# Optimization experiments

Measured on AMD Instinct MI355X. Metric: run time of the kernel, lower is better.

Reference implementation:

```python
import jax, jax.numpy as jnp
import numpy as np

R, B, D, C = 64, 4096, 512, 128  # n_rules, batch, n_fea, n_cls


def setup_inputs() -> dict:
    key = jax.random.key(0)
    k0, k1, k2, k3, k4 = jax.random.split(key, 5)
    x = jax.random.normal(k0, (B, D), dtype=jnp.float32)
    proto = jax.random.normal(k1, (R, D), dtype=jnp.float32)
    var = jax.random.uniform(k2, (R, D), dtype=jnp.float32)
    W = jax.random.normal(k3, (R, D, C), dtype=jnp.float32) * 0.02
    b = jax.random.normal(k4, (R, C), dtype=jnp.float32) * 0.02
    return {"x": x, "proto": proto, "var": var, "W": W, "b": b}


def reference(x, proto, var, W, b):
    # Antecedent: Gaussian membership per rule, var clamped to [1e-4, 0.1]
    v = jnp.clip(var, 0.0001, 0.1)                                  # [R, D]
    diff = x[None, :, :] - proto[:, None, :]                        # [R, B, D]
    m = jnp.exp(-diff * diff / (2.0 * v[:, None, :] ** 2))          # [R, B, D]
    # Firing strength: sum of squared memberships over features, softmax over rules
    fs_ini = jnp.sum(m * m, axis=-1).T                              # [B, R]
    fire_strength = jax.nn.softmax(fs_ini, axis=1)                  # [B, R]
    # Consequent: per-rule Linear + ReLU (batched GEMM over rules)
    expert = jax.nn.relu(jnp.einsum('bd,rdc->rbc', x, W) + b[:, None, :])  # [R, B, C]
    # Softmax-weighted combine over rules
    out = jnp.einsum('rbc,br->bc', expert, fire_strength)           # [B, C]
    return out, fire_strength
```

## Files before the change

kernel.cpp:

```cpp
#include <hip/hip_runtime.h>
#include <hip/hip_bf16.h>
#include <cmath>

#define R_ 64
#define B_ 4096
#define D_ 512
#define C_ 128

typedef __attribute__((ext_vector_type(8))) short bf16x8;
typedef __attribute__((ext_vector_type(4))) float f32x4;

#define VMCNT(n) asm volatile("s_waitcnt vmcnt(" #n ")" ::: "memory")

__device__ __forceinline__ unsigned short f2bf(float f) {
  union { float f; unsigned u; } x; x.f = f;
  unsigned r = (x.u + 0x7FFFu + ((x.u >> 16) & 1u)) >> 16;
  return (unsigned short)r;
}

__global__ void prep_x_kernel(const float* __restrict__ x, unsigned short* __restrict__ xw) {
  int i = blockIdx.x * 256 + threadIdx.x;
  float4 v = reinterpret_cast<const float4*>(x)[i];
  ushort4 o;
  o.x = f2bf(v.x); o.y = f2bf(v.y); o.z = f2bf(v.z); o.w = f2bf(v.w);
  reinterpret_cast<ushort4*>(xw)[i] = o;
}

__global__ void prep_w_kernel(const float* __restrict__ W, unsigned short* __restrict__ wt) {
  __shared__ float t[32][33];
  int bx = blockIdx.x;
  int r = bx >> 6;
  int rem = bx & 63;
  int d0 = (rem >> 2) << 5;
  int c0 = (rem & 3) << 5;
  int tx = threadIdx.x & 31, ty = threadIdx.x >> 5;
  const float* Wr = W + (size_t)r * D_ * C_;
#pragma unroll
  for (int q = 0; q < 4; ++q) {
    int dl = q * 8 + ty;
    t[dl][tx] = Wr[(size_t)(d0 + dl) * C_ + c0 + tx];
  }
  __syncthreads();
  unsigned short* wtr = wt + (size_t)r * C_ * D_;
#pragma unroll
  for (int q = 0; q < 4; ++q) {
    int cl = q * 8 + ty;
    float v = t[tx][cl];
    wtr[(size_t)(c0 + cl) * D_ + d0 + tx] = f2bf(v);
  }
}

__global__ void prep_ps_kernel(const float* __restrict__ proto, const float* __restrict__ var,
                               float* __restrict__ ps) {
  int i = blockIdx.x * 256 + threadIdx.x;
  float v = fminf(fmaxf(var[i], 1e-4f), 0.1f);
  float s = 1.2011224087864498f / v;
  float2 o; o.x = s; o.y = -proto[i] * s;
  reinterpret_cast<float2*>(ps)[i] = o;
}

__global__ __launch_bounds__(256, 4) void fs_partial_kernel(
    const float* __restrict__ x, const float* __restrict__ ps,
    float* __restrict__ fire) {
  __shared__ float x_s[16 * 68];
  __shared__ __align__(16) float ps_s[64 * 128];
  const int tid = threadIdx.x;
  const int b0 = blockIdx.x * 16;
  const int dq = blockIdx.y;

  {
    int row = tid >> 4, c4 = tid & 15;
    float4 v = *reinterpret_cast<const float4*>(&x[(size_t)(b0 + row) * D_ + dq * 64 + c4 * 4]);
    *reinterpret_cast<float4*>(&x_s[row * 68 + c4 * 4]) = v;
  }
#pragma unroll
  for (int k = 0; k < 8; ++k) {
    int g = tid + k * 256;
    int row = g >> 5, gi = g & 31;
    float4 v = *reinterpret_cast<const float4*>(&ps[(size_t)row * (D_ * 2) + dq * 128 + gi * 4]);
    int gs = gi ^ (row & 31);
    *reinterpret_cast<float4*>((char*)ps_s + row * 512 + (gs << 4)) = v;
  }
  __syncthreads();

  const int tr = tid & 63;
  const int tb = tid >> 6;
  const int s31 = tr & 31;
  const char* pb = (const char*)ps_s + tr * 512;
  float facc[4] = {0.f, 0.f, 0.f, 0.f};

#pragma unroll
  for (int d4 = 0; d4 < 16; ++d4) {
    float4 psa = *reinterpret_cast<const float4*>(pb + ((((d4 * 2) ^ s31)) << 4));
    float4 psb = *reinterpret_cast<const float4*>(pb + ((((d4 * 2 + 1) ^ s31)) << 4));
#pragma unroll
    for (int i = 0; i < 4; ++i) {
      float4 xv = *reinterpret_cast<const float4*>(&x_s[(tb * 4 + i) * 68 + d4 * 4]);
      float u0 = fmaf(xv.x, psa.x, psa.y);
      float u1 = fmaf(xv.y, psa.z, psa.w);
      float u2 = fmaf(xv.z, psb.x, psb.y);
      float u3 = fmaf(xv.w, psb.z, psb.w);
      facc[i] += exp2f(-(u0 * u0)) + exp2f(-(u1 * u1)) +
                 exp2f(-(u2 * u2)) + exp2f(-(u3 * u3));
    }
  }
#pragma unroll
  for (int i = 0; i < 4; ++i)
    atomicAdd(&fire[(size_t)(b0 + tb * 4 + i) * R_ + tr], facc[i]);
}

__global__ void softmax_kernel(float* __restrict__ fire) {
  const int b = blockIdx.x * 4 + (threadIdx.x >> 6);
  const int r = threadIdx.x & 63;
  float v = fire[(size_t)b * R_ + r];
  float m = v;
#pragma unroll
  for (int off = 32; off; off >>= 1) m = fmaxf(m, __shfl_xor(m, off, 64));
  float e = exp2f((v - m) * 1.4426950408889634f);
  float s = e;
#pragma unroll
  for (int off = 32; off; off >>= 1) s += __shfl_xor(s, off, 64);
  fire[(size_t)b * R_ + r] = e / s;
}

__global__ __launch_bounds__(512, 2) void gemm_kernel(
    const unsigned short* __restrict__ xw, const unsigned short* __restrict__ wt,
    const float* __restrict__ fire, const float* __restrict__ bias,
    float* __restrict__ out) {
  __shared__ __align__(16) unsigned short x_s[3][256 * 64];
  __shared__ __align__(16) unsigned short w_s[3][128 * 64];
  __shared__ float fire_s[256 * 4];
  __shared__ float bias_s[4 * 128];

  const int tid = threadIdx.x;
  const int rg = blockIdx.x;
  const int bm = blockIdx.y;
  const int b0 = bm * 256;

  {
#pragma unroll
    for (int q = 0; q < 2; ++q) {
      int t = q * 512 + tid;
      int row = t >> 2, g = t & 3;
      fire_s[t] = fire[(size_t)(b0 + row) * R_ + rg * 4 + g];
    }
    bias_s[tid >= 512 ? 0 : tid] = bias[rg * 4 * C_ + tid];
  }

  const int wid = tid >> 6, lane = tid & 63;
  const int wm = wid >> 1, wn = wid & 1;
  const int l16 = lane & 15, lhi = lane >> 4;

  int offA[4][2], offB[4][2];
#pragma unroll
  for (int m = 0; m < 4; ++m) {
    int row = wm * 64 + m * 16 + l16;
#pragma unroll
    for (int ks = 0; ks < 2; ++ks)
      offA[m][ks] = row * 128 + (((ks * 4 + lhi) ^ (row & 7)) << 4);
  }
#pragma unroll
  for (int n = 0; n < 4; ++n) {
    int row = wn * 64 + n * 16 + l16;
#pragma unroll
    for (int ks = 0; ks < 2; ++ks)
      offB[n][ks] = row * 128 + (((ks * 4 + lhi) ^ (row & 7)) << 4);
  }

  int aoff[4], adst[4], boff[2], bdst[2];
#pragma unroll
  for (int q = 0; q < 4; ++q) {
    int ch = q * 512 + tid;
    int row = ch >> 3, g = ch & 7;
    aoff[q] = row * D_ + ((g ^ (row & 7)) << 3);
    adst[q] = ch * 8;
  }
#pragma unroll
  for (int q = 0; q < 2; ++q) {
    int ch = q * 512 + tid;
    int row = ch >> 3, g = ch & 7;
    boff[q] = row * D_ + ((g ^ (row & 7)) << 3);
    bdst[q] = ch * 8;
  }

  const unsigned short* xsrc = xw + (size_t)b0 * D_;
  const unsigned short* wbase = wt + (size_t)(rg * 4) * C_ * D_;

  auto stageA = [&](unsigned short* lds, const unsigned short* src) {
#pragma unroll
    for (int q = 0; q < 4; ++q)
      __builtin_amdgcn_global_load_lds(
          (const __attribute__((address_space(1))) void*)(src + aoff[q]),
          (__attribute__((address_space(3))) void*)(lds + adst[q]), 16, 0, 0);
  };
  auto stageB = [&](unsigned short* lds, const unsigned short* src) {
#pragma unroll
    for (int q = 0; q < 2; ++q)
      __builtin_amdgcn_global_load_lds(
          (const __attribute__((address_space(1))) void*)(src + boff[q]),
          (__attribute__((address_space(3))) void*)(lds + bdst[q]), 16, 0, 0);
  };

  float tot[4][4][4];
#pragma unroll
  for (int m = 0; m < 4; ++m)
#pragma unroll
    for (int n = 0; n < 4; ++n)
#pragma unroll
      for (int j = 0; j < 4; ++j) tot[m][n][j] = 0.f;

  f32x4 acc[4][4];

  stageA(x_s[0], xsrc);
  stageB(w_s[0], wbase);
  stageA(x_s[1], xsrc + 64);
  stageB(w_s[1], wbase + 64);
  VMCNT(6);
  __builtin_amdgcn_s_barrier();

  for (int s = 0; s < 32; ++s) {
    const int g = s >> 3, kk = s & 7;
    if (kk == 0) {
#pragma unroll
      for (int m = 0; m < 4; ++m)
#pragma unroll
        for (int n = 0; n < 4; ++n)
          acc[m][n] = f32x4{0.f, 0.f, 0.f, 0.f};
    }
    if (s + 2 < 32) {
      const int s2 = s + 2;
      unsigned short* xb2 = x_s[s2 % 3];
      unsigned short* wb2 = w_s[s2 % 3];
      stageA(xb2, xsrc + (s2 & 7) * 64);
      stageB(wb2, wbase + (size_t)(s2 >> 3) * C_ * D_ + (s2 & 7) * 64);
    }
    const char* xb = (const char*)x_s[s % 3];
    const char* wb = (const char*)w_s[s % 3];
    bf16x8 av[4][2], bv[4][2];
#pragma unroll
    for (int m = 0; m < 4; ++m)
#pragma unroll
      for (int ks = 0; ks < 2; ++ks)
        av[m][ks] = *reinterpret_cast<const bf16x8*>(xb + offA[m][ks]);
#pragma unroll
    for (int n = 0; n < 4; ++n)
#pragma unroll
      for (int ks = 0; ks < 2; ++ks)
        bv[n][ks] = *reinterpret_cast<const bf16x8*>(wb + offB[n][ks]);
#pragma unroll
    for (int ks = 0; ks < 2; ++ks)
#pragma unroll
      for (int m = 0; m < 4; ++m)
#pragma unroll
        for (int n = 0; n < 4; ++n)
          acc[m][n] = __builtin_amdgcn_mfma_f32_16x16x32_bf16(av[m][ks], bv[n][ks], acc[m][n], 0, 0, 0);
    if (kk == 7) {
#pragma unroll
      for (int m = 0; m < 4; ++m)
#pragma unroll
        for (int n = 0; n < 4; ++n) {
          int col = wn * 64 + n * 16 + l16;
          float bi = bias_s[g * 128 + col];
#pragma unroll
          for (int j = 0; j < 4; ++j) {
            int rowl = wm * 64 + m * 16 + lhi * 4 + j;
            float v = acc[m][n][j] + bi;
            v = fmaxf(v, 0.f);
            tot[m][n][j] += v * fire_s[rowl * 4 + g];
          }
        }
    }
    if (s < 30) { VMCNT(6); }
    else if (s == 30) { VMCNT(0); }
    if (s < 31) __builtin_amdgcn_s_barrier();
  }

#pragma unroll
  for (int m = 0; m < 4; ++m)
#pragma unroll
    for (int n = 0; n < 4; ++n) {
      int col = wn * 64 + n * 16 + l16;
#pragma unroll
      for (int j = 0; j < 4; ++j) {
        int rowl = wm * 64 + m * 16 + lhi * 4 + j;
        atomicAdd(&out[(size_t)(b0 + rowl) * C_ + col], tot[m][n][j]);
      }
    }
}

extern "C" void kernel_launch(void* const* d_in, const int* in_sizes, int n_in,
                              void* d_out, int out_size, void* d_ws, size_t ws_size,
                              hipStream_t stream) {
  const float* x     = (const float*)d_in[0];
  const float* proto = (const float*)d_in[1];
  const float* var   = (const float*)d_in[2];
  const float* W     = (const float*)d_in[3];
  const float* bias  = (const float*)d_in[4];
  float* out  = (float*)d_out;
  float* fire = out + (size_t)B_ * C_;

  const size_t WS_X  = (size_t)B_ * D_ * sizeof(unsigned short);
  const size_t WS_WT = (size_t)R_ * C_ * D_ * sizeof(unsigned short);
  const size_t WS_PS = (size_t)R_ * D_ * 2 * sizeof(float);
  if (ws_size < WS_X + WS_WT + WS_PS) return;

  unsigned short* xw  = (unsigned short*)d_ws;
  unsigned short* wtp = (unsigned short*)((char*)d_ws + WS_X);
  float*          ps  = (float*)((char*)d_ws + WS_X + WS_WT);

  hipMemsetAsync(d_out, 0, (size_t)out_size * sizeof(float), stream);
  prep_x_kernel<<<dim3((B_ * D_ / 4) / 256), dim3(256), 0, stream>>>(x, xw);
  prep_w_kernel<<<dim3(R_ * 64), dim3(256), 0, stream>>>(W, wtp);
  prep_ps_kernel<<<dim3(R_ * D_ / 256), dim3(256), 0, stream>>>(proto, var, ps);
  fs_partial_kernel<<<dim3(B_ / 16, 8), dim3(256), 0, stream>>>(x, ps, fire);
  softmax_kernel<<<dim3(B_ / 4), dim3(256), 0, stream>>>(fire);
  gemm_kernel<<<dim3(16, 16), dim3(512), 0, stream>>>(xw, wtp, fire, bias, out);
}
```

Baseline: 131.7 us.

## Split MFMA k-steps into barrier-synchronized phases with priority boosting

Result: faster. 128.9 us (-2.2%).

```diff
diff --git a/kernel.cpp b/kernel.cpp
--- a/kernel.cpp
+++ b/kernel.cpp
@@ -11,6 +11,7 @@
 typedef __attribute__((ext_vector_type(4))) float f32x4;
 
 #define VMCNT(n) asm volatile("s_waitcnt vmcnt(" #n ")" ::: "memory")
+#define LGKM0()  asm volatile("s_waitcnt lgkmcnt(0)" ::: "memory")
 
 __device__ __forceinline__ unsigned short f2bf(float f) {
   union { float f; unsigned u; } x; x.f = f;
@@ -144,7 +145,7 @@
       int row = t >> 2, g = t & 3;
       fire_s[t] = fire[(size_t)(b0 + row) * R_ + rg * 4 + g];
     }
-    bias_s[tid >= 512 ? 0 : tid] = bias[rg * 4 * C_ + tid];
+    bias_s[tid & 511] = bias[rg * 4 * C_ + (tid & 511)];
   }
 
   const int wid = tid >> 6, lane = tid & 63;
@@ -216,10 +217,13 @@
   stageA(x_s[1], xsrc + 64);
   stageB(w_s[1], wbase + 64);
   VMCNT(6);
+  LGKM0();
   __builtin_amdgcn_s_barrier();
 
   for (int s = 0; s < 32; ++s) {
     const int g = s >> 3, kk = s & 7;
+    const char* xb = (const char*)x_s[s % 3];
+    const char* wb = (const char*)w_s[s % 3];
     if (kk == 0) {
 #pragma unroll
       for (int m = 0; m < 4; ++m)
@@ -227,33 +231,46 @@
         for (int n = 0; n < 4; ++n)
           acc[m][n] = f32x4{0.f, 0.f, 0.f, 0.f};
     }
+    bf16x8 av0[4], bv0[4];
+#pragma unroll
+    for (int m = 0; m < 4; ++m)
+      av0[m] = *reinterpret_cast<const bf16x8*>(xb + offA[m][0]);
+#pragma unroll
+    for (int n = 0; n < 4; ++n)
+      bv0[n] = *reinterpret_cast<const bf16x8*>(wb + offB[n][0]);
     if (s + 2 < 32) {
       const int s2 = s + 2;
-      unsigned short* xb2 = x_s[s2 % 3];
-      unsigned short* wb2 = w_s[s2 % 3];
-      stageA(xb2, xsrc + (s2 & 7) * 64);
-      stageB(wb2, wbase + (size_t)(s2 >> 3) * C_ * D_ + (s2 & 7) * 64);
-    }
-    const char* xb = (const char*)x_s[s % 3];
-    const char* wb = (const char*)w_s[s % 3];
-    bf16x8 av[4][2], bv[4][2];
+      stageA(x_s[s2 % 3], xsrc + (s2 & 7) * 64);
+      stageB(w_s[s2 % 3], wbase + (size_t)(s2 >> 3) * C_ * D_ + (s2 & 7) * 64);
+    }
+    __builtin_amdgcn_s_barrier();
+    LGKM0();
+    __builtin_amdgcn_sched_barrier(0);
+    __builtin_amdgcn_s_setprio(1);
 #pragma unroll
     for (int m = 0; m < 4; ++m)
 #pragma unroll
-      for (int ks = 0; ks < 2; ++ks)
-        av[m][ks] = *reinterpret_cast<const bf16x8*>(xb + offA[m][ks]);
+      for (int n = 0; n < 4; ++n)
+        acc[m][n] = __builtin_amdgcn_mfma_f32_16x16x32_bf16(av0[m], bv0[n], acc[m][n], 0, 0, 0);
+    __builtin_amdgcn_s_setprio(0);
+    __builtin_amdgcn_s_barrier();
+    bf16x8 av1[4], bv1[4];
+#pragma unroll
+    for (int m = 0; m < 4; ++m)
+      av1[m] = *reinterpret_cast<const bf16x8*>(xb + offA[m][1]);
 #pragma unroll
     for (int n = 0; n < 4; ++n)
-#pragma unroll
-      for (int ks = 0; ks < 2; ++ks)
-        bv[n][ks] = *reinterpret_cast<const bf16x8*>(wb + offB[n][ks]);
-#pragma unroll
-    for (int ks = 0; ks < 2; ++ks)
-#pragma unroll
-      for (int m = 0; m < 4; ++m)
-#pragma unroll
-        for (int n = 0; n < 4; ++n)
-          acc[m][n] = __builtin_amdgcn_mfma_f32_16x16x32_bf16(av[m][ks], bv[n][ks], acc[m][n], 0, 0, 0);
+      bv1[n] = *reinterpret_cast<const bf16x8*>(wb + offB[n][1]);
+    __builtin_amdgcn_s_barrier();
+    LGKM0();
+    __builtin_amdgcn_sched_barrier(0);
+    __builtin_amdgcn_s_setprio(1);
+#pragma unroll
+    for (int m = 0; m < 4; ++m)
+#pragma unroll
+      for (int n = 0; n < 4; ++n)
+        acc[m][n] = __builtin_amdgcn_mfma_f32_16x16x32_bf16(av1[m], bv1[n], acc[m][n], 0, 0, 0);
+    __builtin_amdgcn_s_setprio(0);
     if (kk == 7) {
 #pragma unroll
       for (int m = 0; m < 4; ++m)
@@ -270,9 +287,9 @@
           }
         }
     }
-    if (s < 30) { VMCNT(6); }
+    if (s <= 29) { VMCNT(6); }
     else if (s == 30) { VMCNT(0); }
-    if (s < 31) __builtin_amdgcn_s_barrier();
+    __builtin_amdgcn_s_barrier();
   }
 
 #pragma unroll
```
